# Optimization experiments

Measured on AMD Instinct MI355X. Metric: run time of the kernel, lower is better.

The kernel has to match this reference:

```python
import jax, jax.numpy as jnp
import numpy as np

B, T, D_IN, D_H, D_OUT = 32, 2048, 1024, 1024, 1024

def setup_inputs() -> dict:
    key = jax.random.key(0)
    k1, k2, k3, k4, k5 = jax.random.split(key, 5)
    s = jax.random.normal(k1, (B, D_IN), dtype=jnp.float32)
    h = jax.random.normal(k2, (B, T, D_H), dtype=jnp.float32)
    # params (original uses np.random.random, i.e. uniform [0,1); scale kept modest)
    W_a = jax.random.uniform(k3, (D_IN, D_OUT), dtype=jnp.float32)
    U_a = jax.random.uniform(k4, (D_H, D_OUT), dtype=jnp.float32)
    v_a = jax.random.uniform(k5, (D_OUT,), dtype=jnp.float32)
    return {"s": s, "h": h, "W_a": W_a, "U_a": U_a, "v_a": v_a}

def reference(s, h, W_a, U_a, v_a):
    # Bahdanau additive attention:
    # e_bt = v_a . tanh(s W_a + h_t U_a);  a = softmax_t(e);  c_b = sum_t a_bt h_bt
    u_a_h = jnp.einsum('bth,ho->bto', h, U_a)            # [B,T,O]
    w_a_s = jnp.einsum('bi,io->bo', s, W_a)[:, None, :]  # [B,1,O]
    e = jnp.einsum('bto,o->bt', jnp.tanh(w_a_s + u_a_h), v_a)  # [B,T]
    a = jax.nn.softmax(e, axis=-1)                       # [B,T]
    c = jnp.einsum('bt,bth->bh', a, h)                   # [B,H]
    return c
```

## Files before the change

### kernel.cpp

```cpp
#include <hip/hip_runtime.h>
#include <hip/hip_bf16.h>
#include <stdint.h>

#define Bb 32
#define Tt 2048
#define Dd 1024

typedef float    f32x4 __attribute__((ext_vector_type(4)));
typedef _Float16 f16x8 __attribute__((ext_vector_type(8)));
typedef uint32_t u32;

#define WS_A     131072
#define WS_EP    393216
#define WS_UT    4587520

__device__ __forceinline__ void gll16(const void* g, const void* lds) {
  __builtin_amdgcn_global_load_lds(
      (const __attribute__((address_space(1))) u32*)(uintptr_t)g,
      (__attribute__((address_space(3))) u32*)(uint32_t)(uintptr_t)lds,
      16, 0, 0);
}

__global__ __launch_bounds__(256) void k_ws(const float* __restrict__ s,
                                            const float* __restrict__ W,
                                            float* __restrict__ w2_ws) {
  const int b = blockIdx.x >> 2;
  const int o = (blockIdx.x & 3) * 256 + threadIdx.x;
  __shared__ float s_sh[Dd];
#pragma unroll
  for (int j = 0; j < 4; ++j)
    s_sh[threadIdx.x + 256 * j] = s[b * Dd + threadIdx.x + 256 * j];
  __syncthreads();
  float acc = 0.f;
#pragma unroll 8
  for (int i = 0; i < Dd; ++i) acc += s_sh[i] * W[(size_t)i * Dd + o];
  w2_ws[b * Dd + o] = 2.f * acc;
}

__global__ __launch_bounds__(256) void k_ut(const float* __restrict__ U,
                                            uint8_t* __restrict__ U_ts) {
  const int i0 = (blockIdx.x >> 4) * 64;
  const int o0 = (blockIdx.x & 15) * 64;
  __shared__ float tile[64][65];
  const int tx = threadIdx.x & 63;
  const int ty = threadIdx.x >> 6;
#pragma unroll
  for (int jj = 0; jj < 16; ++jj)
    tile[tx][ty + 4 * jj] = U[(size_t)(i0 + ty + 4 * jj) * Dd + o0 + tx];
  __syncthreads();
#pragma unroll
  for (int it = 0; it < 2; ++it) {
    const int g  = it * 256 + threadIdx.x;
    const int ol = g & 63;
    const int kg = g >> 6;
    const int o  = o0 + ol;
    const int k  = i0 + kg * 8;
    f16x8 r;
#pragma unroll
    for (int m = 0; m < 8; ++m) r[m] = (_Float16)tile[ol][kg * 8 + m];
    const int ob  = o >> 7, ks = k >> 6;
    const int o_l = o & 127, k_l = k & 63;
    const size_t byte = ((size_t)(ob * 16 + ks) << 14)
                      + (size_t)((k_l >> 5) * 8192 + (o_l >> 6) * 4096
                      + ((o_l >> 4) & 3) * 1024
                      + (((k_l >> 3) & 3) * 16 + (o_l & 15)) * 16);
    *(f16x8*)(U_ts + byte) = r;
  }
}

__global__ __launch_bounds__(256, 3) void k_e(const float* __restrict__ h,
                                              const uint8_t* __restrict__ U_ts,
                                              const float* __restrict__ w2_ws,
                                              const float* __restrict__ v_a,
                                              float* __restrict__ e_part) {
  const int blk = blockIdx.x;
  const int b   = blk >> 7;
  const int ob  = (blk >> 4) & 7;
  const int tb  = blk & 15;
  const int tid  = threadIdx.x;
  const int lane = tid & 63;
  const int w    = tid >> 6;
  const int hw   = w & 1;
  const int tw   = w >> 1;

  __shared__ __align__(16) uint8_t Al[2][16384];
  __shared__ __align__(16) uint8_t Bl[16384];
  __shared__ float w_sh[128], v_sh[128], exch[128];

  const float* hrow = h + ((size_t)(b * Tt + tb * 128 + (tid >> 3))) * Dd + (tid & 7) * 8;
  int baddr[4];
  {
    const int kk  = (tid & 7) >> 2;
    const int klo = (tid & 7) & 3;
    const int cw  = tid & 7;
#pragma unroll
    for (int j = 0; j < 4; ++j) {
      const int t_l = (tid >> 3) + 32 * j;
      baddr[j] = kk * 8192 + (t_l >> 6) * 4096 + ((t_l >> 4) & 3) * 1024
               + (klo * 16 + ((t_l & 15) ^ cw)) * 16;
    }
  }
  const int klo_r = lane >> 4;
  const int rs0 = (klo_r * 16 + ((lane & 15) ^ klo_r)) * 16;
  const int rs1 = (klo_r * 16 + ((lane & 15) ^ klo_r ^ 4)) * 16;
  const uint8_t* Ub = U_ts + ((size_t)(ob * 16) << 14);

  f32x4 acc[4][4] = {};
  f32x4 br[8];
  f16x8 pk[4];

  if (tid < 128) {
    w_sh[tid] = w2_ws[b * Dd + ob * 128 + tid];
    v_sh[tid] = v_a[ob * 128 + tid];
  }
#pragma unroll
  for (int j = 0; j < 4; ++j) {
    const float* p = hrow + (size_t)j * 32 * Dd;
    br[2 * j]     = *(const f32x4*)p;
    br[2 * j + 1] = *(const f32x4*)(p + 4);
  }
  {
    const uint8_t* As = Ub + (size_t)tid * 16;
    gll16(As,         &Al[0][w * 1024]);
    gll16(As + 4096,  &Al[0][w * 1024 + 4096]);
    gll16(As + 8192,  &Al[0][w * 1024 + 8192]);
    gll16(As + 12288, &Al[0][w * 1024 + 12288]);
  }
#pragma unroll
  for (int j = 0; j < 4; ++j) {
    f16x8 t;
#pragma unroll
    for (int m2 = 0; m2 < 4; ++m2) {
      t[m2]     = (_Float16)br[2 * j][m2];
      t[4 + m2] = (_Float16)br[2 * j + 1][m2];
    }
    pk[j] = t;
  }
  asm volatile("s_waitcnt lgkmcnt(0)" ::: "memory");

#define STEP(KS, CUR, PRE, VMC)                                               \
  {                                                                           \
    __builtin_amdgcn_sched_barrier(0);                                        \
    __builtin_amdgcn_s_barrier();                   \
    __builtin_amdgcn_sched_barrier(0);                                        \
    _Pragma("unroll")                                                         \
    for (int j = 0; j < 4; ++j) *(f16x8*)(Bl + baddr[j]) = pk[j];             \
    if (PRE) {                                                                \
      _Pragma("unroll")                            \
      for (int j = 0; j < 4; ++j) {                                           \
        const float* p = hrow + (size_t)j * 32 * Dd + ((KS) + 1) * 64;        \
        br[2 * j]     = *(const f32x4*)p;                                     \
        br[2 * j + 1] = *(const f32x4*)(p + 4);                               \
      }                                                                       \
      const uint8_t* As = Ub + ((size_t)((KS) + 1) << 14) + (size_t)tid * 16; \
      gll16(As,         &Al[(CUR) ^ 1][w * 1024]);                            \
      gll16(As + 4096,  &Al[(CUR) ^ 1][w * 1024 + 4096]);                     \
      gll16(As + 8192,  &Al[(CUR) ^ 1][w * 1024 + 8192]);                     \
      gll16(As + 12288, &Al[(CUR) ^ 1][w * 1024 + 12288]);                    \
    }                                                                         \
    asm volatile("s_waitcnt lgkmcnt(0)" ::: "memory");    \
    asm volatile(VMC ::: "memory");                     \
    __builtin_amdgcn_sched_barrier(0);                                        \
    __builtin_amdgcn_s_barrier();                                     \
    __builtin_amdgcn_sched_barrier(0);                                        \
    _Pragma("unroll")                                                         \
    for (int kk = 0; kk < 2; ++kk) {                                          \
      f16x8 af[4], bf[4];                                                     \
      _Pragma("unroll")                                                       \
      for (int n = 0; n < 4; ++n)                                             \
        af[n] = *(const f16x8*)(&Al[CUR][0] + kk * 8192 + hw * 4096           \
                                + n * 1024 + lane * 16);                      \
      _Pragma("unroll")                                                       \
      for (int m = 0; m < 4; ++m)                                             \
        bf[m] = *(const f16x8*)(Bl + kk * 8192 + tw * 4096 + m * 1024         \
                                + (kk ? rs1 : rs0));                          \
      _Pragma("unroll")                                                       \
      for (int m = 0; m < 4; ++m)                                             \
        _Pragma("unroll")                                                     \
        for (int n = 0; n < 4; ++n)                                           \
          acc[m][n] = __builtin_amdgcn_mfma_f32_16x16x32_f16(af[n], bf[m],    \
                                                             acc[m][n], 0, 0, 0); \
    }                                                                         \
    if (PRE) {                                   \
      __builtin_amdgcn_sched_barrier(0);                                      \
      _Pragma("unroll")                                                       \
      for (int j = 0; j < 4; ++j) {                                           \
        f16x8 t;                                                              \
        _Pragma("unroll")                                                     \
        for (int m2 = 0; m2 < 4; ++m2) {                                      \
          t[m2]     = (_Float16)br[2 * j][m2];                                \
          t[4 + m2] = (_Float16)br[2 * j + 1][m2];                            \
        }                                                                     \
        pk[j] = t;                                                            \
      }                                                                       \
    }                                                                         \
  }

#pragma unroll 1
  for (int ks2 = 0; ks2 < 7; ++ks2) {
    const int ks = ks2 * 2;
    STEP(ks,     0, 1, "s_waitcnt vmcnt(12)")
    STEP(ks + 1, 1, 1, "s_waitcnt vmcnt(12)")
  }
  STEP(14, 0, 1, "s_waitcnt vmcnt(12)")
  STEP(15, 1, 0, "s_waitcnt vmcnt(0)")
#undef STEP

  float ep[4] = {0.f, 0.f, 0.f, 0.f};
#pragma unroll
  for (int m = 0; m < 4; ++m)
#pragma unroll
    for (int n = 0; n < 4; ++n)
#pragma unroll
      for (int r = 0; r < 4; ++r) {
        const int o_loc = hw * 64 + n * 16 + ((lane >> 4) << 2) + r;
        const float x = __builtin_fmaf(acc[m][n][r], 2.f, w_sh[o_loc]);
        ep[m] += v_sh[o_loc] * (1.f - 2.f / (__expf(x) + 1.f));
      }
#pragma unroll
  for (int m = 0; m < 4; ++m) {
    ep[m] += __shfl_xor(ep[m], 16, 64);
    ep[m] += __shfl_xor(ep[m], 32, 64);
  }
  __syncthreads();
  if (hw == 1 && lane < 16) {
#pragma unroll
    for (int m = 0; m < 4; ++m) exch[tw * 64 + m * 16 + lane] = ep[m];
  }
  __syncthreads();
  if (hw == 0 && lane < 16) {
#pragma unroll
    for (int m = 0; m < 4; ++m) {
      const int t_loc = tw * 64 + m * 16 + lane;
      e_part[((size_t)(ob * Bb + b)) * Tt + tb * 128 + t_loc] = ep[m] + exch[t_loc];
    }
  }
}

__global__ __launch_bounds__(256) void k_sm(const float* __restrict__ e_part,
                                            float* __restrict__ a_ws) {
  const int b = blockIdx.x;
  const int lane = threadIdx.x & 63;
  const int wv = threadIdx.x >> 6;
  __shared__ float red[8];
  float ev[8];
  float m = -1e30f;
#pragma unroll
  for (int j = 0; j < 8; ++j) {
    const int t = threadIdx.x + 256 * j;
    float sv = 0.f;
#pragma unroll
    for (int o = 0; o < 8; ++o) sv += e_part[((size_t)(o * Bb + b)) * Tt + t];
    ev[j] = sv;
    m = fmaxf(m, sv);
  }
#pragma unroll
  for (int sft = 1; sft < 64; sft <<= 1) m = fmaxf(m, __shfl_xor(m, sft, 64));
  if (lane == 0) red[wv] = m;
  __syncthreads();
  m = fmaxf(fmaxf(red[0], red[1]), fmaxf(red[2], red[3]));
  float sum = 0.f;
#pragma unroll
  for (int j = 0; j < 8; ++j) { ev[j] = __expf(ev[j] - m); sum += ev[j]; }
#pragma unroll
  for (int sft = 1; sft < 64; sft <<= 1) sum += __shfl_xor(sum, sft, 64);
  if (lane == 0) red[4 + wv] = sum;
  __syncthreads();
  const float inv = 1.f / (red[4] + red[5] + red[6] + red[7]);
#pragma unroll
  for (int j = 0; j < 8; ++j) a_ws[b * Tt + threadIdx.x + 256 * j] = ev[j] * inv;
}

__global__ __launch_bounds__(256) void k_c1(const float* __restrict__ h,
                                            const float* __restrict__ a_ws,
                                            float* __restrict__ cpart) {
  const int b  = blockIdx.x >> 5;
  const int tc = blockIdx.x & 31;
  const int t0 = tc << 6;
  __shared__ float a_sh[64];
  if (threadIdx.x < 64) a_sh[threadIdx.x] = a_ws[b * Tt + t0 + threadIdx.x];
  __syncthreads();
  f32x4 acc = {0.f, 0.f, 0.f, 0.f};
  const float* hb = h + ((size_t)b * Tt + t0) * Dd + threadIdx.x * 4;
#pragma unroll 4
  for (int t = 0; t < 64; ++t) {
    const f32x4 hv = *(const f32x4*)(hb + (size_t)t * Dd);
    acc += a_sh[t] * hv;
  }
  *(f32x4*)(cpart + ((size_t)(tc * 32 + b) << 10) + threadIdx.x * 4) = acc;
}

__global__ __launch_bounds__(256) void k_c2(const float* __restrict__ cpart,
                                            float* __restrict__ out) {
  const int gid = blockIdx.x * 256 + threadIdx.x;
  const int b = gid >> 10;
  const int d = gid & 1023;
  float sv = 0.f;
#pragma unroll
  for (int tc = 0; tc < 32; ++tc) sv += cpart[((size_t)(tc * 32 + b) << 10) + d];
  out[gid] = sv;
}

extern "C" void kernel_launch(void* const* d_in, const int* in_sizes, int n_in,
                              void* d_out, int out_size, void* d_ws, size_t ws_size,
                              hipStream_t stream) {
  (void)in_sizes; (void)n_in; (void)out_size; (void)ws_size;
  const float* s  = (const float*)d_in[0];
  const float* h  = (const float*)d_in[1];
  const float* W  = (const float*)d_in[2];
  const float* U  = (const float*)d_in[3];
  const float* v  = (const float*)d_in[4];
  uint8_t* ws = (uint8_t*)d_ws;
  float*   w2_ws  = (float*)ws;
  float*   a_ws   = (float*)(ws + WS_A);
  float*   e_part = (float*)(ws + WS_EP);
  float*   cpart  = (float*)(ws + WS_EP);
  uint8_t* U_ts   = ws + WS_UT;

  k_ws<<<128, 256, 0, stream>>>(s, W, w2_ws);
  k_ut<<<256, 256, 0, stream>>>(U, U_ts);
  k_e <<<4096, 256, 0, stream>>>(h, U_ts, w2_ws, v, e_part);
  k_sm<<<Bb, 256, 0, stream>>>(e_part, a_ws);
  k_c1<<<1024, 256, 0, stream>>>(h, a_ws, cpart);
  k_c2<<<128, 256, 0, stream>>>(cpart, (float*)d_out);
}
```

Before: 296.4 us.

## Deepen k_e pipeline with double-buffered B tile and two-stage h prefetch

Restructures the k_e main loop so the h rows are prefetched two k-steps ahead into alternating register sets, and the converted fp16 B tile is double-buffered in LDS. This leaves one barrier per step instead of two and gives global loads more time to land before they are consumed. In exchange it doubles B LDS usage and adds register pressure, so launch bounds drop from 3 to 2 blocks per SIMD, lowering occupancy.

```diff
diff --git a/kernel.cpp b/kernel.cpp
--- a/kernel.cpp
+++ b/kernel.cpp
@@ -68,7 +68,7 @@
   }
 }
 
-__global__ __launch_bounds__(256, 3) void k_e(const float* __restrict__ h,
+__global__ __launch_bounds__(256, 2) void k_e(const float* __restrict__ h,
                                               const uint8_t* __restrict__ U_ts,
                                               const float* __restrict__ w2_ws,
                                               const float* __restrict__ v_a,
@@ -84,7 +84,7 @@
   const int tw   = w >> 1;
 
   __shared__ __align__(16) uint8_t Al[2][16384];
-  __shared__ __align__(16) uint8_t Bl[16384];
+  __shared__ __align__(16) uint8_t Bl[2 * 16384];
   __shared__ float w_sh[128], v_sh[128], exch[128];
 
   const float* hrow = h + ((size_t)(b * Tt + tb * 128 + (tid >> 3))) * Dd + (tid & 7) * 8;
@@ -106,7 +106,7 @@
   const uint8_t* Ub = U_ts + ((size_t)(ob * 16) << 14);
 
   f32x4 acc[4][4] = {};
-  f32x4 br[8];
+  f32x4 brA[8], brB[8];
   f16x8 pk[4];
 
   if (tid < 128) {
@@ -116,8 +116,14 @@
 #pragma unroll
   for (int j = 0; j < 4; ++j) {
     const float* p = hrow + (size_t)j * 32 * Dd;
-    br[2 * j]     = *(const f32x4*)p;
-    br[2 * j + 1] = *(const f32x4*)(p + 4);
+    brA[2 * j]     = *(const f32x4*)p;
+    brA[2 * j + 1] = *(const f32x4*)(p + 4);
+  }
+#pragma unroll
+  for (int j = 0; j < 4; ++j) {
+    const float* p = hrow + (size_t)j * 32 * Dd + 64;
+    brB[2 * j]     = *(const f32x4*)p;
+    brB[2 * j + 1] = *(const f32x4*)(p + 4);
   }
   {
     const uint8_t* As = Ub + (size_t)tid * 16;
@@ -131,49 +137,68 @@
     f16x8 t;
 #pragma unroll
     for (int m2 = 0; m2 < 4; ++m2) {
-      t[m2]     = (_Float16)br[2 * j][m2];
-      t[4 + m2] = (_Float16)br[2 * j + 1][m2];
+      t[m2]     = (_Float16)brA[2 * j][m2];
+      t[4 + m2] = (_Float16)brA[2 * j + 1][m2];
+    }
+    *(f16x8*)(Bl + baddr[j]) = t;
+  }
+#pragma unroll
+  for (int j = 0; j < 4; ++j) {
+    f16x8 t;
+#pragma unroll
+    for (int m2 = 0; m2 < 4; ++m2) {
+      t[m2]     = (_Float16)brB[2 * j][m2];
+      t[4 + m2] = (_Float16)brB[2 * j + 1][m2];
     }
     pk[j] = t;
   }
+#pragma unroll
+  for (int j = 0; j < 4; ++j) {
+    const float* p = hrow + (size_t)j * 32 * Dd + 128;
+    brA[2 * j]     = *(const f32x4*)p;
+    brA[2 * j + 1] = *(const f32x4*)(p + 4);
+  }
   asm volatile("s_waitcnt lgkmcnt(0)" ::: "memory");
 
-#define STEP(KS, CUR, PRE, VMC)                                               \
+#define STEP(KS, BRL, BRC, DO_LD, DO_CVT, DO_ST, VMC)                         \
   {                                                                           \
+    asm volatile(VMC ::: "memory");                                           \
     __builtin_amdgcn_sched_barrier(0);                                        \
-    __builtin_amdgcn_s_barrier();                   \
+    __builtin_amdgcn_s_barrier();                                             \
     __builtin_amdgcn_sched_barrier(0);                                        \
-    _Pragma("unroll")                                                         \
-    for (int j = 0; j < 4; ++j) *(f16x8*)(Bl + baddr[j]) = pk[j];             \
-    if (PRE) {                                                                \
-      _Pragma("unroll")                            \
+    const int cur_ = (KS) & 1;                                                \
+    if (DO_ST) {                                                              \
+      const int nb_ = cur_ ^ 1;                                               \
+      const uint8_t* As = Ub + ((size_t)((KS) + 1) << 14) + (size_t)tid * 16; \
+      gll16(As,         &Al[nb_][w * 1024]);                                  \
+      gll16(As + 4096,  &Al[nb_][w * 1024 + 4096]);                           \
+      gll16(As + 8192,  &Al[nb_][w * 1024 + 8192]);                           \
+      gll16(As + 12288, &Al[nb_][w * 1024 + 12288]);                          \
+      __builtin_amdgcn_sched_barrier(0);          \
+      _Pragma("unroll")                                                       \
+      for (int j = 0; j < 4; ++j)                                             \
+        *(f16x8*)(Bl + nb_ * 16384 + baddr[j]) = pk[j];                       \
+    }                                                                         \
+    if (DO_LD) {                                                              \
+      _Pragma("unroll")                                                       \
       for (int j = 0; j < 4; ++j) {                                           \
-        const float* p = hrow + (size_t)j * 32 * Dd + ((KS) + 1) * 64;        \
-        br[2 * j]     = *(const f32x4*)p;                                     \
-        br[2 * j + 1] = *(const f32x4*)(p + 4);                               \
+        const float* p = hrow + (size_t)j * 32 * Dd + ((KS) + 3) * 64;        \
+        BRL[2 * j]     = *(const f32x4*)p;                                    \
+        BRL[2 * j + 1] = *(const f32x4*)(p + 4);                              \
       }                                                                       \
-      const uint8_t* As = Ub + ((size_t)((KS) + 1) << 14) + (size_t)tid * 16; \
-      gll16(As,         &Al[(CUR) ^ 1][w * 1024]);                            \
-      gll16(As + 4096,  &Al[(CUR) ^ 1][w * 1024 + 4096]);                     \
-      gll16(As + 8192,  &Al[(CUR) ^ 1][w * 1024 + 8192]);                     \
-      gll16(As + 12288, &Al[(CUR) ^ 1][w * 1024 + 12288]);                    \
     }                                                                         \
-    asm volatile("s_waitcnt lgkmcnt(0)" ::: "memory");    \
-    asm volatile(VMC ::: "memory");                     \
-    __builtin_amdgcn_sched_barrier(0);                                        \
-    __builtin_amdgcn_s_barrier();                                     \
-    __builtin_amdgcn_sched_barrier(0);                                        \
+    __builtin_amdgcn_sched_barrier(0);          \
     _Pragma("unroll")                                                         \
     for (int kk = 0; kk < 2; ++kk) {                                          \
       f16x8 af[4], bf[4];                                                     \
       _Pragma("unroll")                                                       \
       for (int n = 0; n < 4; ++n)                                             \
-        af[n] = *(const f16x8*)(&Al[CUR][0] + kk * 8192 + hw * 4096           \
+        af[n] = *(const f16x8*)(&Al[cur_][0] + kk * 8192 + hw * 4096          \
                                 + n * 1024 + lane * 16);                      \
       _Pragma("unroll")                                                       \
       for (int m = 0; m < 4; ++m)                                             \
-        bf[m] = *(const f16x8*)(Bl + kk * 8192 + tw * 4096 + m * 1024         \
-                                + (kk ? rs1 : rs0));                          \
+        bf[m] = *(const f16x8*)(Bl + cur_ * 16384 + kk * 8192 + tw * 4096     \
+                                + m * 1024 + (kk ? rs1 : rs0));               \
       _Pragma("unroll")                                                       \
       for (int m = 0; m < 4; ++m)                                             \
         _Pragma("unroll")                                                     \
@@ -181,29 +206,32 @@
           acc[m][n] = __builtin_amdgcn_mfma_f32_16x16x32_f16(af[n], bf[m],    \
                                                              acc[m][n], 0, 0, 0); \
     }                                                                         \
-    if (PRE) {                                   \
-      __builtin_amdgcn_sched_barrier(0);                                      \
+    if (DO_CVT) {                                                             \
+      __builtin_amdgcn_sched_barrier(0);      \
       _Pragma("unroll")                                                       \
       for (int j = 0; j < 4; ++j) {                                           \
         f16x8 t;                                                              \
         _Pragma("unroll")                                                     \
         for (int m2 = 0; m2 < 4; ++m2) {                                      \
-          t[m2]     = (_Float16)br[2 * j][m2];                                \
-          t[4 + m2] = (_Float16)br[2 * j + 1][m2];                            \
+          t[m2]     = (_Float16)BRC[2 * j][m2];                               \
+          t[4 + m2] = (_Float16)BRC[2 * j + 1][m2];                           \
         }                                                                     \
         pk[j] = t;                                                            \
       }                                                                       \
     }                                                                         \
+    asm volatile("s_waitcnt lgkmcnt(0)" ::: "memory");        \
   }
 
 #pragma unroll 1
-  for (int ks2 = 0; ks2 < 7; ++ks2) {
+  for (int ks2 = 0; ks2 < 6; ++ks2) {
     const int ks = ks2 * 2;
-    STEP(ks,     0, 1, "s_waitcnt vmcnt(12)")
-    STEP(ks + 1, 1, 1, "s_waitcnt vmcnt(12)")
-  }
-  STEP(14, 0, 1, "s_waitcnt vmcnt(12)")
-  STEP(15, 1, 0, "s_waitcnt vmcnt(0)")
+    STEP(ks,     brB, brA, 1, 1, 1, "s_waitcnt vmcnt(8)")
+    STEP(ks + 1, brA, brB, 1, 1, 1, "s_waitcnt vmcnt(8)")
+  }
+  STEP(12, brB, brA, 1, 1, 1, "s_waitcnt vmcnt(8)")
+  STEP(13, brA, brB, 0, 1, 1, "s_waitcnt vmcnt(8)")
+  STEP(14, brA, brB, 0, 0, 1, "s_waitcnt vmcnt(0)")
+  STEP(15, brA, brB, 0, 0, 0, "s_waitcnt vmcnt(0)")
 #undef STEP
 
   float ep[4] = {0.f, 0.f, 0.f, 0.f};
```

Measured after the change: 305.5 us. +3.1%, slower.
